# Performance work log

Measured on AMD Instinct MI355X. Metric: run time of the kernel, lower is better.

The kernel has to match this reference:

```python
import jax, jax.numpy as jnp
import numpy as np
from jax.scipy.special import logsumexp

# static problem sizes (all graphs identical size; pairs interleaved [q0,c0,q1,c1,...])
B = 64; NG = 2 * B; N = 48; E = 192; MAX_N = 64; MAX_E = 256
D_IN = 32; D = 128; EDGE_EMB = 128; M = 256; S = 64
T = 5; K = 3; TEMP = 0.1; SINK_ITERS = 10
VN = NG * N; VE = NG * E


def _mlp2(x, W1, b1, W2, b2):
    return jnp.maximum(x @ W1 + b1, 0.0) @ W2 + b2


def setup_inputs():
    keys = iter(jax.random.split(jax.random.key(0), 64))
    def w(fan_in, fan_out):
        return jax.random.normal(next(keys), (fan_in, fan_out), dtype=jnp.float32) * (1.0 / float(np.sqrt(fan_in)))
    z = lambda n: jnp.zeros((n,), jnp.float32)
    inp = {}
    inp['node_features'] = jax.random.normal(next(keys), (VN, D_IN), dtype=jnp.float32)
    inp['edge_features'] = jax.random.normal(next(keys), (VE, D_IN), dtype=jnp.float32)
    off = jnp.repeat(jnp.arange(NG, dtype=jnp.int32) * N, E)
    inp['from_idx'] = jax.random.randint(next(keys), (VE,), 0, N, dtype=jnp.int32) + off
    inp['to_idx'] = jax.random.randint(next(keys), (VE,), 0, N, dtype=jnp.int32) + off
    inp['enc_node_W'] = w(D_IN, D); inp['enc_node_b'] = z(D)
    inp['enc_edge_W'] = w(D_IN, EDGE_EMB); inp['enc_edge_b'] = z(EDGE_EMB)
    inp['ni_W1'] = w(2 * D, 2 * D); inp['ni_b1'] = z(2 * D)
    inp['ni_W2'] = w(2 * D, D); inp['ni_b2'] = z(D)
    ei_in = M + EDGE_EMB
    inp['ei_W1'] = w(ei_in, ei_in); inp['ei_b1'] = z(ei_in)
    inp['ei_W2'] = w(ei_in, EDGE_EMB); inp['ei_b2'] = z(EDGE_EMB)
    inp['msg_W'] = w(2 * D + EDGE_EMB, M); inp['msg_b'] = z(M)
    inp['nu_W1'] = w(D + M, 2 * D); inp['nu_b1'] = z(2 * D)
    inp['nu_W2'] = w(2 * D, D); inp['nu_b2'] = z(D)
    inp['ns_W1'] = w(D, S); inp['ns_b1'] = z(S)
    inp['ns_W2'] = w(S, S); inp['ns_b2'] = z(S)
    inp['es_W1'] = w(M, S); inp['es_b1'] = z(S)
    inp['es_W2'] = w(S, S); inp['es_b2'] = z(S)
    return inp


def _forward(node_features, edge_features, enc_node_W, enc_node_b, enc_edge_W, enc_edge_b,
             ni_W1, ni_b1, ni_W2, ni_b2, ei_W1, ei_b1, ei_W2, ei_b2, msg_W, msg_b,
             nu_W1, nu_b1, nu_W2, nu_b2, ns_W1, ns_b1, ns_W2, ns_b2,
             es_W1, es_b1, es_W2, es_b2, from_idx, to_idx):
    enc_n = node_features @ enc_node_W + enc_node_b            # [VN, D]
    enc_e = edge_features @ enc_edge_W + enc_edge_b            # [VE, EDGE_EMB]
    node_store = jnp.zeros((VN, D * (T + 1)), jnp.float32)
    edge_store = jnp.zeros((VE, M * (T + 1)), jnp.float32)
    # flat index of node/edge j of graph g inside interleaved padded store: g*max + j
    node_pad_idx = (jnp.arange(NG)[:, None] * MAX_N + jnp.arange(N)[None, :]).reshape(-1)
    edge_pad_idx = (jnp.arange(NG)[:, None] * MAX_E + jnp.arange(E)[None, :]).reshape(-1)
    node_mask = (jnp.arange(MAX_N) < N).astype(jnp.float32)[None, :, None]
    edge_mask = (jnp.arange(MAX_E) < E).astype(jnp.float32)[None, :, None]

    def transport(store, n_per, max_set, fdim, sW1, sb1, sW2, sb2, mask):
        x = store.reshape(NG, n_per, store.shape[-1])
        x = jnp.pad(x, ((0, 0), (0, max_set - n_per), (0, 0)))   # pad to max set size
        q, c = x[0::2], x[1::2]                                   # [B, max, dim_total]
        fq, fc = q[:, :, -fdim:], c[:, :, -fdim:]
        tq = _mlp2(fq, sW1, sb1, sW2, sb2) * mask
        tc = _mlp2(fc, sW1, sb1, sW2, sb2) * mask
        la = jnp.einsum('bqs,bcs->bqc', tq, tc) / TEMP
        for _ in range(SINK_ITERS):
            la = la - logsumexp(la, axis=2, keepdims=True)
            la = la - logsumexp(la, axis=1, keepdims=True)
        plan = jnp.exp(la)
        qi = jnp.einsum('bqc,bcd->bqd', plan, c)                  # query <- corpus
        ci = jnp.einsum('bqc,bqd->bcd', plan, q)                  # corpus <- query
        inter = jnp.stack([qi, ci], axis=1).reshape(NG * max_set, -1)
        return plan, inter, fq, fc

    for _ in range(K):  # time_update_steps
        h, e = enc_n, enc_e
        node_slots = [jnp.zeros((VN, D), jnp.float32)]
        edge_slots = [jnp.zeros((VE, M), jnp.float32)]
        for p in range(1, T + 1):  # propagation_steps
            h_comb = _mlp2(jnp.concatenate([h, node_store[:, (p - 1) * D:p * D]], -1), ni_W1, ni_b1, ni_W2, ni_b2)
            e_comb = _mlp2(jnp.concatenate([e, edge_store[:, (p - 1) * M:p * M]], -1), ei_W1, ei_b1, ei_W2, ei_b2)
            src, dst = h_comb[from_idx], h_comb[to_idx]
            fwd_msg = jnp.concatenate([src, dst, e_comb], -1) @ msg_W + msg_b
            bwd_msg = jnp.concatenate([dst, src, e_comb], -1) @ msg_W + msg_b
            agg = jax.ops.segment_sum(fwd_msg, to_idx, num_segments=VN) + jax.ops.segment_sum(bwd_msg, from_idx, num_segments=VN)
            h = _mlp2(jnp.concatenate([h_comb, agg], -1), nu_W1, nu_b1, nu_W2, nu_b2)
            src2, dst2 = h[from_idx], h[to_idx]
            msgs = (jnp.concatenate([src2, dst2, e_comb], -1) @ msg_W + msg_b) + \
                   (jnp.concatenate([dst2, src2, e_comb], -1) @ msg_W + msg_b)
            node_slots.append(h)
            edge_slots.append(msgs)
        upd_node = jnp.concatenate(node_slots, axis=1)
        upd_edge = jnp.concatenate(edge_slots, axis=1)
        n_plan, n_inter, ffq, ffc = transport(upd_node, N, MAX_N, D, ns_W1, ns_b1, ns_W2, ns_b2, node_mask)
        _, e_inter, _, _ = transport(upd_edge, E, MAX_E, M, es_W1, es_b1, es_W2, es_b2, edge_mask)
        node_store = jnp.concatenate([jnp.zeros((VN, D), jnp.float32), n_inter[node_pad_idx, D:]], axis=1)
        edge_store = jnp.concatenate([jnp.zeros((VE, M), jnp.float32), e_inter[edge_pad_idx, M:]], axis=1)

    # feature_alignment_score: -sum relu(q - P c)
    score = -jnp.sum(jnp.maximum(ffq - jnp.einsum('bqc,bcd->bqd', n_plan, ffc), 0.0), axis=(1, 2))
    return score


def reference(node_features, edge_features, from_idx, to_idx, enc_node_W, enc_node_b, enc_edge_W, enc_edge_b,
              ni_W1, ni_b1, ni_W2, ni_b2, ei_W1, ei_b1, ei_W2, ei_b2, msg_W, msg_b,
              nu_W1, nu_b1, nu_W2, nu_b2, ns_W1, ns_b1, ns_W2, ns_b2,
              es_W1, es_b1, es_W2, es_b2):
    return _forward(node_features, edge_features, enc_node_W, enc_node_b, enc_edge_W, enc_edge_b,
                    ni_W1, ni_b1, ni_W2, ni_b2, ei_W1, ei_b1, ei_W2, ei_b2, msg_W, msg_b,
                    nu_W1, nu_b1, nu_W2, nu_b2, ns_W1, ns_b1, ns_W2, ns_b2,
                    es_W1, es_b1, es_W2, es_b2, from_idx, to_idx)
```

## Files before the change

### kernel.cpp

```cpp
#include <hip/hip_runtime.h>
#include <cstdint>
#include <cstddef>

#define NGg   128
#define Bb    64
#define Nn    48
#define Ee    192
#define Sdim  64
#define VNn   6144
#define VEe   24576
#define INV_TEMP 10.0f
#define ADJ_STRIDE 96

typedef unsigned short u16;
typedef unsigned int   u32;
typedef __attribute__((ext_vector_type(8))) short short8;
typedef __attribute__((ext_vector_type(4))) float floatx4;

__device__ __forceinline__ u16 f2bf(float f)
{
    unsigned int u = __float_as_uint(f);
    u += 0x7FFFu + ((u >> 16) & 1u);
    return (u16)(u >> 16);
}
// ... 233 lines not shown
            for (int q = 0; q < 8; q++) {
                hi[q] = __builtin_amdgcn_perm(pk[2 * q + 1], pk[2 * q], 0x05040100u);
                lo[q] = __builtin_amdgcn_perm(pk[2 * q + 1], pk[2 * q], 0x07060302u);
            }
            *(uint4*)&Ah[srow * TW + skoff]     = ((uint4*)hi)[0];
            *(uint4*)&Ah[srow * TW + skoff + 8] = ((uint4*)hi)[1];
            *(uint4*)&Al[srow * TW + skoff]     = ((uint4*)lo)[0];
            *(uint4*)&Al[srow * TW + skoff + 8] = ((uint4*)lo)[1];
        }
        __syncthreads();
        short8 afh[4], afl[4], bfh[4], bfl[4];
        #pragma unroll
        for (int i = 0; i < 4; i++) {
            const int ro = (wm * 64 + i * 16 + l15) * TW + lq * 8;
            afh[i] = *(const short8*)&Ah[ro];
            afl[i] = *(const short8*)&Al[ro];
        }
        #pragma unroll
        for (int j = 0; j < 4; j++) {
            const int ro = (wn * 64 + j * 16 + l15) * TW + lq * 8;
            bfh[j] = *(const short8*)&Bh[ro];
            bfl[j] = *(const short8*)&Bl[ro];
        }
        #pragma unroll
        for (int i = 0; i < 4; i++)
            #pragma unroll
            for (int j = 0; j < 4; j++) {
                acc[i][j] = __builtin_amdgcn_mfma_f32_16x16x32_bf16(afh[i], bfl[j], acc[i][j], 0, 0, 0);
                acc[i][j] = __builtin_amdgcn_mfma_f32_16x16x32_bf16(afl[i], bfh[j], acc[i][j], 0, 0, 0);
                acc[i][j] = __builtin_amdgcn_mfma_f32_16x16x32_bf16(afh[i], bfh[j], acc[i][j], 0, 0, 0);
            }
        __syncthreads();
    }
    if (d.flags & FL_MSGS) {
        #pragma unroll
        for (int i = 0; i < 4; i++) {
            #pragma unroll
            for (int r = 0; r < 4; r++) {
                const int row = bm + wm * 64 + i * 16 + lq * 4 + r;
                const int fi = d.fidx[row], ti = d.tidx[row];
                #pragma unroll
                for (int j = 0; j < 4; j++) {
                    const int col = bn + wn * 64 + j * 16 + l15;
                    float v = 2.f * (acc[i][j][r] + d.bias[col])
                            + d.qs[(size_t)fi * 256 + col] + d.qs[(size_t)ti * 256 + col];
                    ((u32*)d.C)[(size_t)row * d.ldc + col] = packhl(v);
                }
            }
        }
        return;
    }
    const int relu = d.flags & FL_RELU;
    const int opk  = d.flags & FL_OUTPK;
    #pragma unroll
    for (int j = 0; j < 4; j++) {
        const int col = bn + wn * 64 + j * 16 + l15;
        const bool cok = (col < d.Ncap);
        const float bv = (d.bias && cok) ? d.bias[col] : 0.f;
        #pragma unroll
        for (int i = 0; i < 4; i++) {
            const int row0 = bm + wm * 64 + i * 16 + lq * 4;
            #pragma unroll
            for (int r = 0; r < 4; r++) {
                float v = acc[i][j][r] + bv;
                if (relu) v = fmaxf(v, 0.f);
                if (cok) {
                    if (opk)
                        ((u32*)d.C)[(size_t)(row0 + r) * d.ldc + col] = packhl(v);
                    else
                        ((float*)d.C)[(size_t)(row0 + r) * d.ldc + col] = v;
                }
            }
        }
    }
}

static inline void gemm2(hipStream_t s, const GemmDesc& d0, const GemmDesc& d1)
{
    gemm2_pk_kernel<<<d0.nblk + d1.nblk, 256, 0, s>>>(d0, d1, d0.nblk);
}
static inline void gemm1(hipStream_t s, const GemmDesc& d0)
{
    gemm2_pk_kernel<<<d0.nblk, 256, 0, s>>>(d0, d0, d0.nblk);
}

__global__ __launch_bounds__(256) void gemm_f32_kernel(
    const float* __restrict__ A, int lda, int K,
    const u16* __restrict__ Wh, const u16* __restrict__ Wl, int ldwt,
    const float* __restrict__ bias, u32* __restrict__ C, int ldc, int Ncap)
{
    __shared__ __align__(16) u16 Ah[128 * TW];
    __shared__ __align__(16) u16 Al[128 * TW];
    __shared__ __align__(16) u16 Bh[128 * TW];
    __shared__ __align__(16) u16 Bl[128 * TW];
    const int tid = threadIdx.x;
    const int lane = tid & 63, wave = tid >> 6;
    const int wm = wave >> 1, wn = wave & 1;
    const int bm = blockIdx.y * 128, bn = blockIdx.x * 128;
    const int srow = tid >> 1;
    const int skoff = (tid & 1) * 16;
    const int arow = bm + srow, brow = bn + srow;
    const int l15 = lane & 15, lq = lane >> 4;

    floatx4 acc[4][4];
    #pragma unroll
    for (int i = 0; i < 4; i++)
        #pragma unroll
        for (int j = 0; j < 4; j++) acc[i][j] = (floatx4){0.f, 0.f, 0.f, 0.f};

    for (int k0 = 0; k0 < K; k0 += 32) {
        const int kk = k0 + skoff;
        const float* asrc = A + (size_t)arow * lda + kk;
        float f[16];
        ((float4*)f)[0] = ((const float4*)asrc)[0];
        ((float4*)f)[1] = ((const float4*)asrc)[1];
        ((float4*)f)[2] = ((const float4*)asrc)[2];
        ((float4*)f)[3] = ((const float4*)asrc)[3];
        u16 ph[16], pl8[16];
        #pragma unroll
        for (int q = 0; q < 16; q++) {
            u16 h = f2bf(f[q]);
            ph[q] = h;
            pl8[q] = f2bf(f[q] - bf2f(h));
        }
        *(uint4*)&Ah[srow * TW + skoff]     = *(const uint4*)&ph[0];
        *(uint4*)&Ah[srow * TW + skoff + 8] = *(const uint4*)&ph[8];
        *(uint4*)&Al[srow * TW + skoff]     = *(const uint4*)&pl8[0];
        *(uint4*)&Al[srow * TW + skoff + 8] = *(const uint4*)&pl8[8];
        const u16* bh = Wh + (size_t)brow * ldwt + kk;
        const u16* bl = Wl + (size_t)brow * ldwt + kk;
        *(uint4*)&Bh[srow * TW + skoff]     = ((const uint4*)bh)[0];
        *(uint4*)&Bh[srow * TW + skoff + 8] = ((const uint4*)bh)[1];
        *(uint4*)&Bl[srow * TW + skoff]     = ((const uint4*)bl)[0];
        *(uint4*)&Bl[srow * TW + skoff + 8] = ((const uint4*)bl)[1];
        __syncthreads();
        short8 afh[4], afl[4], bfh[4], bfl[4];
        #pragma unroll
        for (int i = 0; i < 4; i++) {
            const int ro = (wm * 64 + i * 16 + l15) * TW + lq * 8;
            afh[i] = *(const short8*)&Ah[ro];
            afl[i] = *(const short8*)&Al[ro];
        }
        #pragma unroll
        for (int j = 0; j < 4; j++) {
            const int ro = (wn * 64 + j * 16 + l15) * TW + lq * 8;
            bfh[j] = *(const short8*)&Bh[ro];
            bfl[j] = *(const short8*)&Bl[ro];
        }
        #pragma unroll
        for (int i = 0; i < 4; i++)
            #pragma unroll
            for (int j = 0; j < 4; j++) {
                acc[i][j] = __builtin_amdgcn_mfma_f32_16x16x32_bf16(afh[i], bfl[j], acc[i][j], 0, 0, 0);
                acc[i][j] = __builtin_amdgcn_mfma_f32_16x16x32_bf16(afl[i], bfh[j], acc[i][j], 0, 0, 0);
                acc[i][j] = __builtin_amdgcn_mfma_f32_16x16x32_bf16(afh[i], bfh[j], acc[i][j], 0, 0, 0);
            }
        __syncthreads();
    }
    #pragma unroll
    for (int j = 0; j < 4; j++) {
        const int col = bn + wn * 64 + j * 16 + l15;
        const bool cok = (col < Ncap);
        const float bv = cok ? bias[col] : 0.f;
        #pragma unroll
        for (int i = 0; i < 4; i++) {
            const int row0 = bm + wm * 64 + i * 16 + lq * 4;
// ... 92 lines not shown
                } else {
                    #pragma unroll
                    for (int i = 0; i < 8; i++)
                        pk[i] = Pb[(size_t)(k0 + sak + i) * ms + m];
                }
                #pragma unroll
                for (int i = 0; i < 8; i++)
                    if (k0 + sak + i >= n_per) pk[i] = 0;
            } else {
                #pragma unroll
                for (int i = 0; i < 8; i++) pk[i] = 0;
            }
            u32 hi[4], lo[4];
            #pragma unroll
            for (int q = 0; q < 4; q++) {
                hi[q] = __builtin_amdgcn_perm(pk[2 * q + 1], pk[2 * q], 0x05040100u);
                lo[q] = __builtin_amdgcn_perm(pk[2 * q + 1], pk[2 * q], 0x07060302u);
            }
            *(uint4*)&Ah[sar * TW + sak] = *(uint4*)hi;
            *(uint4*)&Al[sar * TW + sak] = *(uint4*)lo;
        }
        {
            u16 qh[16], ql[16];
            #pragma unroll
            for (int i = 0; i < 16; i++) {
                int kk = k0 + sbk + i;
                u32 w = 0;
                if (kk < n_per) w = U[(size_t)(ibase + kk) * ldu + bn + sbn];
                qh[i] = (u16)w; ql[i] = (u16)(w >> 16);
            }
            *(uint4*)&Bh[sbn * TW + sbk]     = *(const uint4*)&qh[0];
            *(uint4*)&Bh[sbn * TW + sbk + 8] = *(const uint4*)&qh[8];
            *(uint4*)&Bl[sbn * TW + sbk]     = *(const uint4*)&ql[0];
            *(uint4*)&Bl[sbn * TW + sbk + 8] = *(const uint4*)&ql[8];
        }
        __syncthreads();
        short8 afh[2], afl[2], bfh[4], bfl[4];
        #pragma unroll
        for (int i = 0; i < 2; i++) {
            const int ro = (wm * 32 + i * 16 + l15) * TW + lq * 8;
            afh[i] = *(const short8*)&Ah[ro];
            afl[i] = *(const short8*)&Al[ro];
        }
        #pragma unroll
        for (int j = 0; j < 4; j++) {
            const int ro = (wn * 64 + j * 16 + l15) * TW + lq * 8;
            bfh[j] = *(const short8*)&Bh[ro];
            bfl[j] = *(const short8*)&Bl[ro];
        }
        #pragma unroll
        for (int i = 0; i < 2; i++)
            #pragma unroll
            for (int j = 0; j < 4; j++) {
                acc[i][j] = __builtin_amdgcn_mfma_f32_16x16x32_bf16(afh[i], bfl[j], acc[i][j], 0, 0, 0);
                acc[i][j] = __builtin_amdgcn_mfma_f32_16x16x32_bf16(afl[i], bfh[j], acc[i][j], 0, 0, 0);
                acc[i][j] = __builtin_amdgcn_mfma_f32_16x16x32_bf16(afh[i], bfh[j], acc[i][j], 0, 0, 0);
            }
        __syncthreads();
    }
    #pragma unroll
    for (int j = 0; j < 4; j++) {
        const int col = bn + wn * 64 + j * 16 + l15;
        #pragma unroll
        for (int i = 0; i < 2; i++) {
            const int row0 = bm + wm * 32 + i * 16 + lq * 4;
            #pragma unroll
            for (int r = 0; r < 4; r++) {
                const int m = row0 + r;
                if (m < n_per)
                    C[(size_t)(obase + m) * ldc + col] = packhl(acc[i][j][r]);
            }
        }
    }
}

static inline void bgemmDual(hipStream_t s, const u32* P, int ms, int n_per,
                             const u32* U, int ldu, u32* C, int ldc, int N)
{
    int nxh = N / 128;
    dim3 grid(nxh * 2, (n_per + 63) / 64, Bb);
    bgemm_dual_kernel<<<grid, 256, 0, s>>>(P, ms, n_per, U, ldu, C, ldc, nxh);
}

__global__ __launch_bounds__(256) void la_sinkhorn64_kernel(
    const float* __restrict__ tt, u32* __restrict__ n_la)
{
    const int b = blockIdx.x;
    __shared__ float Aq[64][65];
    __shared__ float Ac[64][65];
    __shared__ float m[64][65];
    __shared__ float v_s[64];
    __shared__ float part[4][64];
    const int tid = threadIdx.x;
    const int lane = tid & 63, w = tid >> 6;
    for (int idx = tid; idx < 4096; idx += 256) {
        int r = idx >> 6, s = idx & 63;
        float vq = 0.f, vc = 0.f;
        if (r < Nn) {
            vq = tt[((size_t)(2 * b) * Nn + r) * Sdim + s];
            vc = tt[((size_t)(2 * b + 1) * Nn + r) * Sdim + s];
        }
        Aq[r][s] = vq;
        Ac[r][s] = vc;
    }
    __syncthreads();
    {
        const int tx = tid & 15, ty = tid >> 4;
        float acc[4][4] = {};
        for (int s = 0; s < 64; s++) {
            float a[4], c[4];
            #pragma unroll
            for (int i = 0; i < 4; i++) a[i] = Aq[ty * 4 + i][s];
            #pragma unroll
            for (int j = 0; j < 4; j++) c[j] = Ac[tx * 4 + j][s];
            #pragma unroll
            for (int i = 0; i < 4; i++)
                #pragma unroll
                for (int j = 0; j < 4; j++)
                    acc[i][j] = fmaf(a[i], c[j], acc[i][j]);
        }
        #pragma unroll
        for (int i = 0; i < 4; i++)
            #pragma unroll
            for (int j = 0; j < 4; j++)
                m[ty * 4 + i][tx * 4 + j] = acc[i][j] * INV_TEMP;
    }
    if (tid < 64) v_s[tid] = 0.f;
    __syncthreads();
    float x[16], u[16];
    #pragma unroll
    for (int j = 0; j < 16; j++) x[j] = m[w * 16 + j][lane];
    #pragma unroll
    for (int j = 0; j < 16; j++) {
        float mx = x[j];
        #pragma unroll
        for (int d = 1; d < 64; d <<= 1) mx = fmaxf(mx, __shfl_xor(mx, d));
        u[j] = mx;
    }
    for (int it = 0; it < 10; it++) {
        float vr = v_s[lane];
        #pragma unroll
        for (int j = 0; j < 16; j++) {
            float s = __expf(x[j] - vr - u[j]);
            #pragma unroll
            for (int d = 1; d < 64; d <<= 1) s += __shfl_xor(s, d);
            u[j] += __logf(s);
        }
        float s = 0.f;
        #pragma unroll
        for (int j = 0; j < 16; j++) s += __expf(x[j] - u[j] - vr);
        part[w][lane] = s;
        __syncthreads();
        if (tid < 64) {
            float ss = part[0][tid] + part[1][tid] + part[2][tid] + part[3][tid];
            v_s[tid] += __logf(ss);
        }
        __syncthreads();
    }
    float vr = v_s[lane];
    u32* g = n_la + (size_t)b * 4096;
    #pragma unroll
    for (int j = 0; j < 16; j++)
        g[(size_t)(w * 16 + j) * 64 + lane] = packhl(__expf(x[j] - u[j] - vr));
}

__global__ __launch_bounds__(256) void la_gemm256_kernel(
    const float* __restrict__ tt, float* __restrict__ la)
{
    const int b = blockIdx.z;
    const int bm = blockIdx.y * 64, bn = blockIdx.x * 64;
    __shared__ float Aq[64][65];
    __shared__ float Ac[64][65];
    const int tid = threadIdx.x;
    for (int idx = tid; idx < 4096; idx += 256) {
        int r = idx >> 6, s = idx & 63;
        float vq = 0.f, vc = 0.f;
        int qr = bm + r, cr = bn + r;
        if (qr < Ee) vq = tt[((size_t)(2 * b) * Ee + qr) * Sdim + s];
        if (cr < Ee) vc = tt[((size_t)(2 * b + 1) * Ee + cr) * Sdim + s];
        Aq[r][s] = vq;
        Ac[r][s] = vc;
    }
    __syncthreads();
    const int tx = tid & 15, ty = tid >> 4;
    float acc[4][4] = {};
    for (int s = 0; s < 64; s++) {
        float a[4], c[4];
        #pragma unroll
        for (int i = 0; i < 4; i++) a[i] = Aq[ty * 4 + i][s];
        #pragma unroll
        for (int j = 0; j < 4; j++) c[j] = Ac[tx * 4 + j][s];
        #pragma unroll
        for (int i = 0; i < 4; i++)
            #pragma unroll
            for (int j = 0; j < 4; j++)
                acc[i][j] = fmaf(a[i], c[j], acc[i][j]);
    }
    #pragma unroll
    for (int i = 0; i < 4; i++)
        #pragma unroll
        for (int j = 0; j < 4; j++)
            la[((size_t)b * 256 + bm + ty * 4 + i) * 256 + bn + tx * 4 + j] = acc[i][j] * INV_TEMP;
}

__global__ __launch_bounds__(1024, 4) void sinkhorn256_kernel(float* __restrict__ la)
{
    const int b = blockIdx.x;
    float* g = la + (size_t)b * 65536;
    const int tid = threadIdx.x;
    const int lane = tid & 63, w = tid >> 6;
    __shared__ float v_s[256];
    __shared__ float part[16][64][5];

    float4 x[16];
    float u[16];
    #pragma unroll
    for (int j = 0; j < 16; j++) {
        x[j] = ((const float4*)(g + (size_t)(w * 16 + j) * 256))[lane];
        float mx = fmaxf(fmaxf(x[j].x, x[j].y), fmaxf(x[j].z, x[j].w));
        #pragma unroll
        for (int d = 1; d < 64; d <<= 1) mx = fmaxf(mx, __shfl_xor(mx, d));
        u[j] = mx;
    }
    if (tid < 256) v_s[tid] = 0.f;
    __syncthreads();

    for (int it = 0; it < 10; it++) {
        const float4 vr = *(const float4*)&v_s[4 * lane];
        float cp0 = 0.f, cp1 = 0.f, cp2 = 0.f, cp3 = 0.f;
        #pragma unroll
        for (int j = 0; j < 16; j++) {
            float e0 = __expf(x[j].x - vr.x - u[j]);
            float e1 = __expf(x[j].y - vr.y - u[j]);
            float e2 = __expf(x[j].z - vr.z - u[j]);
            float e3 = __expf(x[j].w - vr.w - u[j]);
            float s = e0 + e1 + e2 + e3;
            #pragma unroll
            for (int d = 1; d < 64; d <<= 1) s += __shfl_xor(s, d);
            u[j] += __logf(s);
            const float inv = 1.f / s;
            cp0 = fmaf(e0, inv, cp0);
            cp1 = fmaf(e1, inv, cp1);
            cp2 = fmaf(e2, inv, cp2);
            cp3 = fmaf(e3, inv, cp3);
        }
        *(float4*)&part[w][lane][0] = (float4){cp0, cp1, cp2, cp3};
        __syncthreads();
        if (tid < 256) {
            const int cl = tid >> 2, cq = tid & 3;
            float ss = 0.f;
            #pragma unroll
            for (int w2 = 0; w2 < 16; w2++) ss += part[w2][cl][cq];
            v_s[tid] += __logf(ss);
        }
        __syncthreads();
    }
    const float4 vr = *(const float4*)&v_s[4 * lane];
    #pragma unroll
    for (int j = 0; j < 16; j++) {
        u32 o[4];
        o[0] = packhl(__expf(x[j].x - u[j] - vr.x));
        o[1] = packhl(__expf(x[j].y - u[j] - vr.y));
        o[2] = packhl(__expf(x[j].z - u[j] - vr.z));
        o[3] = packhl(__expf(x[j].w - u[j] - vr.w));
        ((uint4*)(g + (size_t)(w * 16 + j) * 256))[lane] = *(uint4*)o;
    }
}

__global__ __launch_bounds__(256) void zero_deg_kernel(int* __restrict__ deg)
{
    deg[blockIdx.x * 256 + threadIdx.x] = 0;
}

__global__ __launch_bounds__(256) void csr_build_kernel(
    const int* __restrict__ from_idx, const int* __restrict__ to_idx,
    int* __restrict__ deg, u32* __restrict__ adj)
{
    int e = blockIdx.x * 256 + threadIdx.x;
    if (e >= VEe) return;
    int f = from_idx[e], t = to_idx[e];
    int p1 = atomicAdd(&deg[t], 1);
    if (p1 < ADJ_STRIDE) adj[(size_t)t * ADJ_STRIDE + p1] = ((u32)e << 13) | (u32)f;
    int p2 = atomicAdd(&deg[f], 1);
    if (p2 < ADJ_STRIDE) adj[(size_t)f * ADJ_STRIDE + p2] = ((u32)e << 13) | (u32)t;
}

__global__ __launch_bounds__(256) void agg_csr_kernel(
    const u32* __restrict__ P01,
    const u32* __restrict__ ec2,
    const int* __restrict__ deg, const u32* __restrict__ adj,
    u32* __restrict__ agg)
{
    const int n = blockIdx.x;
    const int d = threadIdx.x;
    __shared__ u32 sadj[ADJ_STRIDE];
    __shared__ int sdeg;
    if (d == 0) sdeg = min(deg[n], ADJ_STRIDE);
    if (d < ADJ_STRIDE) sadj[d] = adj[(size_t)n * ADJ_STRIDE + d];
    __syncthreads();
    const int dn = sdeg;
    float a = (float)dn * unpackhl(P01[(size_t)n * 512 + 256 + d]);
    for (int i = 0; i < dn; i++) {
        const u32 en = sadj[i];
        const int e = (int)(en >> 13), pr = (int)(en & 8191u);
        a += unpackhl(ec2[(size_t)e * 256 + d]) + unpackhl(P01[(size_t)pr * 512 + d]);
    }
    agg[(size_t)n * 256 + d] = packhl(a);
}

__global__ __launch_bounds__(256) void msgs_inplace_kernel(
    u32* __restrict__ m, const float* __restrict__ Qs,
    const int* __restrict__ from_idx, const int* __restrict__ to_idx)
{
    const int e = blockIdx.x;
    const int d = threadIdx.x;
    const int f = from_idx[e], t = to_idx[e];
    size_t o = (size_t)e * 256 + d;
    float v = Qs[(size_t)f * 256 + d] + Qs[(size_t)t * 256 + d] + 2.f * unpackhl(m[o]);
    m[o] = packhl(v);
}

__global__ void diag_kernel(float* __restrict__ out, float v)
{
    out[threadIdx.x] = v;
}

__global__ __launch_bounds__(128) void score_kernel(
    const u32* __restrict__ upd_node, const u32* __restrict__ plan,
    float* __restrict__ out)
{
    const int b = blockIdx.x;
    const int tid = threadIdx.x;
    __shared__ float ffc[48][128];
    __shared__ float pl[64][48];
    __shared__ float red[128];
    for (int c = 0; c < 48; c++)
        ffc[c][tid] = unpackhl(upd_node[(size_t)((2 * b + 1) * 48 + c) * 640 + 512 + tid]);
    for (int idx = tid; idx < 64 * 48; idx += 128) {
        int q = idx / 48, c = idx % 48;
        pl[q][c] = unpackhl(plan[(size_t)b * 4096 + q * 64 + c]);
    }
    __syncthreads();
    float accv = 0.f;
    for (int q = 0; q < 64; q++) {
        float rsum = 0.f;
        #pragma unroll 8
        for (int c = 0; c < 48; c++) rsum = fmaf(pl[q][c], ffc[c][tid], rsum);
        float fq = 0.f;
        if (q < 48) fq = unpackhl(upd_node[(size_t)((2 * b) * 48 + q) * 640 + 512 + tid]);
        accv += fmaxf(fq - rsum, 0.f);
    }
    red[tid] = accv;
    __syncthreads();
    for (int sft = 64; sft > 0; sft >>= 1) {
        if (tid < sft) red[tid] += red[tid + sft];
        __syncthreads();
    }
    if (tid == 0) out[b] = -red[0];
}

#define OFF_UPD_NODE   0ULL
#define OFF_NODE_STORE 3932160ULL
#define OFF_EDGE_STORE 7077888ULL
#define OFF_ECOMB      32243712ULL
#define OFF_ENC_N      47972352ULL
#define OFF_ENC_E      48758784ULL
#define OFF_N_LA       51904512ULL
#define OFF_WT         52199424ULL
#define OFF_WTL        52547584ULL
#define OFF_ARENA      52895744ULL
#define OFF_DEG        66265088ULL
#define OFF_ADJ        66271232ULL
#define TOTAL_FLOATS   66861056ULL

#define WT_NIW1   0
#define WT_NIW2   65536
#define WT_EIW1   98304
#define WT_EIW2   245760
#define WT_MSG    294912
#define WT_P01    393216
#define WT_NUW1   458752
#define WT_NUW2   557056
#define WT_WSUM   589824
#define WT_ENCN   622592
#define WT_ENCE   626688
#define WT_NS1    630784
#define WT_NS2    647168
#define WT_ES1    655360
#define WT_ES2    688128

#define PK(p) ((u32*)(p))

extern "C" void kernel_launch(void* const* d_in, const int* in_sizes, int n_in,
                              void* d_out, int out_size, void* d_ws, size_t ws_size,
                              hipStream_t stream)
{
    (void)in_sizes; (void)n_in; (void)out_size;
    if (ws_size < TOTAL_FLOATS * sizeof(float)) {
        diag_kernel<<<1, 64, 0, stream>>>((float*)d_out, (float)ws_size);
        return;
    }

// ... 34 lines not shown
    float* edge_store = ws + OFF_EDGE_STORE;
    float* ecomb      = ws + OFF_ECOMB;
    float* enc_n      = ws + OFF_ENC_N;
    float* enc_e      = ws + OFF_ENC_E;
    float* n_la       = ws + OFF_N_LA;
    u16* WT  = (u16*)(ws + OFF_WT);
    u16* WTL = (u16*)(ws + OFF_WTL);
    float* arena      = ws + OFF_ARENA;
    int* deg = (int*)(ws + OFF_DEG);
    u32* adj = (u32*)(ws + OFF_ADJ);

    float* A_hidden = arena;
    float* A_hcomb  = arena + 1572864;
    float* A_ehid   = arena + 2359296;
    float* A_ec2    = arena + 2359296;
    float* A_P01    = arena + 8650752;
    float* A_aggb   = arena + 11796480;
    float* B_Qs       = arena;
    float* B_Qs2      = ecomb + (size_t)4 * VEe * 128;
    float* B_thid_e   = arena + 8650752;
    float* B_ttreal_e = arena + 10223616;
    float* B_ela      = arena + 2359296;
    float* B_msgs     = arena + 6553600;
    float* B_thid_n   = arena + 12058624;
    float* B_ttreal_n = arena + 12451840;

    prep_kernel<<<(696320 + 255) / 256, 256, 0, stream>>>(
        ni_W1, ni_W2, ei_W1, ei_W2, msg_W, nu_W1, nu_W2,
        enc_node_W, enc_edge_W, ns_W1, ns_W2, es_W1, es_W2, WT, WTL);
    zero_deg_kernel<<<VNn / 256, 256, 0, stream>>>(deg);
    csr_build_kernel<<<VEe / 256, 256, 0, stream>>>(from_idx, to_idx, deg, adj);

    gemm_f32_kernel<<<dim3(1, VNn / 128), 256, 0, stream>>>(
        node_features, 32, 32, WT + WT_ENCN, WTL + WT_ENCN, 32, enc_node_b, PK(enc_n), 128, 128);
    gemm_f32_kernel<<<dim3(1, VEe / 128), 256, 0, stream>>>(
        edge_features, 32, 32, WT + WT_ENCE, WTL + WT_ENCE, 32, enc_edge_b, PK(enc_e), 128, 128);

    for (int k = 0; k < 3; k++) {
        for (int p = 1; p <= 5; p++) {
            const bool hs = (k > 0) && (p > 1);
            const u32* hA1 = (p == 1) ? PK(enc_n) : PK(upd_node + (size_t)(p - 2) * 128);
            const int  hlda1 = (p == 1) ? 128 : 640;
            const u32* hA2 = hs ? PK(node_store + (size_t)(p - 2) * 128) : nullptr;
            const int  hK2 = hs ? 128 : 0;
            GemmDesc hcomb1_d = mkDesc(hA1, hlda1, 128, hA2, 512, hK2,
                                       WT + WT_NIW1, WTL + WT_NIW1, 256, ni_b1,
                                       A_hidden, 256, VNn, 256, 256, FL_RELU | FL_OUTPK);
            GemmDesc hcomb2_d = mkDesc(PK(A_hidden), 256, 256, nullptr, 0, 0,
                                       WT + WT_NIW2, WTL + WT_NIW2, 256, ni_b2,
                                       A_hcomb, 128, VNn, 128, 128, FL_OUTPK);
            GemmDesc p01_d = mkDesc(PK(A_hcomb), 128, 128, nullptr, 0, 0,
                                    WT + WT_P01, WTL + WT_P01, 128, nullptr,
                                    A_P01, 512, VNn, 512, 512, FL_OUTPK);

            const bool edge_full = ((k == 0 && p == 1) || (k > 0 && p > 1));
            if (edge_full) {
                const u32* esrc = (k == 0) ? nullptr : PK(edge_store + (size_t)(p - 2) * 256);
                const int  eK2  = (k == 0) ? 0 : 256;
                float* ec_slot = (k == 0) ? ecomb : ecomb + (size_t)(p - 1) * VEe * 128;
                GemmDesc eiW1_d = mkDesc(PK(enc_e), 128, 128, esrc, 1024, eK2,
                                         WT + WT_EIW1, WTL + WT_EIW1, 384, ei_b1,
                                         A_ehid, 384, VEe, 384, 384, FL_RELU | FL_OUTPK);
                GemmDesc eiW2_d = mkDesc(PK(A_ehid), 384, 384, nullptr, 0, 0,
                                         WT + WT_EIW2, WTL + WT_EIW2, 384, ei_b2,
                                         ec_slot, 128, VEe, 128, 128, FL_OUTPK);
                GemmDesc ec2_d = mkDesc(PK(ec_slot), 128, 128, nullptr, 0, 0,
                                        WT + WT_MSG + 256, WTL + WT_MSG + 256, 384, msg_b,
                                        A_ec2, 256, VEe, 256, 256, FL_OUTPK);
                gemm2(stream, eiW1_d, hcomb1_d);
                gemm2(stream, eiW2_d, hcomb2_d);
                gemm2(stream, ec2_d, p01_d);
            } else if (k > 0 && p == 1) {
                GemmDesc ec2_d = mkDesc(PK(ecomb), 128, 128, nullptr, 0, 0,
                                        WT + WT_MSG + 256, WTL + WT_MSG + 256, 384, msg_b,
                                        A_ec2, 256, VEe, 256, 256, FL_OUTPK);
                gemm2(stream, ec2_d, hcomb1_d);
                gemmPK(stream, 64, 64, PK(A_hidden), 256, 256, nullptr, 0, 0,
                       WT + WT_NIW2, WTL + WT_NIW2, 256,
                       ni_b2, A_hcomb, 128, VNn, 128, 128, FL_OUTPK);
                gemmPK(stream, 64, 128, PK(A_hcomb), 128, 128, nullptr, 0, 0,
                       WT + WT_P01, WTL + WT_P01, 128,
                       nullptr, A_P01, 512, VNn, 512, 512, FL_OUTPK);
            } else {
                gemmPK(stream, 64, 128, hA1, hlda1, 128, hA2, 512, hK2,
                       WT + WT_NIW1, WTL + WT_NIW1, 256, ni_b1,
                       A_hidden, 256, VNn, 256, 256, FL_RELU | FL_OUTPK);
                gemmPK(stream, 64, 64, PK(A_hidden), 256, 256, nullptr, 0, 0,
                       WT + WT_NIW2, WTL + WT_NIW2, 256,
                       ni_b2, A_hcomb, 128, VNn, 128, 128, FL_OUTPK);
                gemmPK(stream, 64, 128, PK(A_hcomb), 128, 128, nullptr, 0, 0,
                       WT + WT_P01, WTL + WT_P01, 128,
                       nullptr, A_P01, 512, VNn, 512, 512, FL_OUTPK);
            }
            agg_csr_kernel<<<VNn, 256, 0, stream>>>(PK(A_P01), PK(A_ec2), deg, adj, PK(A_aggb));
            gemmPK(stream, 64, 128, PK(A_hcomb), 128, 128, PK(A_aggb), 256, 256,
                   WT + WT_NUW1, WTL + WT_NUW1, 384,
                   nu_b1, A_hidden, 256, VNn, 256, 256, FL_RELU | FL_OUTPK);
            gemmPK(stream, 64, 64, PK(A_hidden), 256, 256, nullptr, 0, 0,
                   WT + WT_NUW2, WTL + WT_NUW2, 256,
                   nu_b2, upd_node + (size_t)(p - 1) * 128, 640, VNn, 128, 128, FL_OUTPK);
        }
        if (k < 2) {
            gemmPK(stream, 64, 128, PK(upd_node + 512), 640, 128, nullptr, 0, 0,
                   WT + WT_WSUM, WTL + WT_WSUM, 128,
                   nullptr, B_Qs, 256, VNn, 256, 256, 0);
            msgs_inplace_kernel<<<VEe, 256, 0, stream>>>(PK(A_ec2), B_Qs, from_idx, to_idx);
            GemmDesc es1_d = mkDesc(PK(A_ec2), 256, 256, nullptr, 0, 0,
                                    WT + WT_ES1, WTL + WT_ES1, 256, es_b1,
                                    B_thid_e, 64, VEe, 128, 64, FL_RELU | FL_OUTPK);
            GemmDesc ns1_d = mkDesc(PK(upd_node + 512), 640, 128, nullptr, 0, 0,
                                    WT + WT_NS1, WTL + WT_NS1, 128, ns_b1,
                                    B_thid_n, 64, VNn, 128, 64, FL_RELU | FL_OUTPK);
            gemm2(stream, es1_d, ns1_d);
            GemmDesc es2_d = mkDesc(PK(B_thid_e), 64, 64, nullptr, 0, 0,
                                    WT + WT_ES2, WTL + WT_ES2, 64, es_b2,
                                    B_ttreal_e, 64, VEe, 128, 64, 0);
            GemmDesc ns2_d = mkDesc(PK(B_thid_n), 64, 64, nullptr, 0, 0,
                                    WT + WT_NS2, WTL + WT_NS2, 64, ns_b2,
                                    B_ttreal_n, 64, VNn, 128, 64, 0);
            gemm2(stream, es2_d, ns2_d);
            la_sinkhorn64_kernel<<<Bb, 256, 0, stream>>>(B_ttreal_n, PK(n_la));
            la_gemm256_kernel<<<dim3(4, 4, Bb), 256, 0, stream>>>(B_ttreal_e, B_ela);
            sinkhorn256_kernel<<<Bb, 1024, 0, stream>>>(B_ela);
            bgemmDual(stream, PK(n_la), 64, 48, PK(upd_node), 640, PK(node_store), 512, 512);
            float* qsbuf[2] = { B_Qs2, B_Qs };
            GemmDesc qs1_d = mkDesc(PK(upd_node), 640, 128, nullptr, 0, 0,
                                    WT + WT_WSUM, WTL + WT_WSUM, 128, nullptr,
                                    qsbuf[0], 256, VNn, 256, 256, 0);
            gemm1(stream, qs1_d);
            for (int sl = 1; sl <= 4; sl++) {
                const size_t ss = (k == 0) ? 0 : (size_t)(sl - 1);
                GemmDesc em_d = mkDesc(PK(ecomb + ss * VEe * 128), 128, 128, nullptr, 0, 0,
                                       WT + WT_MSG + 256, WTL + WT_MSG + 256, 384, msg_b,
                                       B_msgs, 256, VEe, 256, 256, FL_MSGS);
                em_d.qs = qsbuf[(sl - 1) & 1];
                em_d.fidx = from_idx; em_d.tidx = to_idx;
                if (sl < 4) {
                    GemmDesc qsn_d = mkDesc(PK(upd_node + (size_t)sl * 128), 640, 128,
                                            nullptr, 0, 0,
                                            WT + WT_WSUM, WTL + WT_WSUM, 128, nullptr,
                                            qsbuf[sl & 1], 256, VNn, 256, 256, 0);
                    gemm2(stream, em_d, qsn_d);
                } else {
                    gemm1(stream, em_d);
                }
                bgemmDual(stream, PK(B_ela), 256, 192, PK(B_msgs), 256,
                          PK(edge_store + (size_t)(sl - 1) * 256), 1024, 256);
            }
        } else {
            gemmPK(stream, 64, 64, PK(upd_node + 512), 640, 128, nullptr, 0, 0,
                   WT + WT_NS1, WTL + WT_NS1, 128,
                   ns_b1, B_thid_n, 64, VNn, 64, 64, FL_RELU | FL_OUTPK);
            gemmPK(stream, 64, 64, PK(B_thid_n), 64, 64, nullptr, 0, 0,
                   WT + WT_NS2, WTL + WT_NS2, 64,
                   ns_b2, B_ttreal_n, 64, VNn, 64, 64, 0);
            la_sinkhorn64_kernel<<<Bb, 256, 0, stream>>>(B_ttreal_n, PK(n_la));
        }
    }
    score_kernel<<<Bb, 128, 0, stream>>>(PK(upd_node), PK(n_la), (float*)d_out);
}
```

Measured before the change: 2.916 ms.

## Fuse message construction into ES1 GEMM, merge LA kernels, retune tiles

Adds a dedicated GEMM kernel that builds the edge message (Qs[from]+Qs[to]+2*ec2) on the fly while loading A tiles, which removes the separate in-place message kernel and its full read/write pass over the edge buffer. The Qs GEMM is now batched with the NS1 GEMM in one launch. The node Sinkhorn and edge logit GEMM kernels are merged into one launch distinguished by block index. The 256 Sinkhorn kernel now re-reads rows from global memory each iteration instead of holding them in registers, and drops its occupancy hint, trading memory traffic for register pressure. Some node GEMM tile widths change from 128 to 64.

```diff
diff --git a/kernel.cpp b/kernel.cpp
--- a/kernel.cpp
+++ b/kernel.cpp
@@ -339,6 +339,111 @@
 static inline void gemm1(hipStream_t s, const GemmDesc& d0)
 {
     gemm2_pk_kernel<<<d0.nblk, 256, 0, s>>>(d0, d0, d0.nblk);
+}
+
+__global__ __launch_bounds__(256) void gemm_es1msgs_kernel(
+    const u32* __restrict__ A,
+    const float* __restrict__ qs,
+    const int* __restrict__ fidx, const int* __restrict__ tidx,
+    const u16* __restrict__ Wh, const u16* __restrict__ Wl,
+    const float* __restrict__ bias,
+    u32* __restrict__ C)
+{
+    __shared__ __align__(16) u16 Ah[128 * TW];
+    __shared__ __align__(16) u16 Al[128 * TW];
+    __shared__ __align__(16) u16 Bh[64 * TW];
+    __shared__ __align__(16) u16 Bl[64 * TW];
+    const int tid = threadIdx.x;
+    const int lane = tid & 63, wave = tid >> 6;
+    const int wm = wave >> 1, wn = wave & 1;
+    const int bm = blockIdx.y * 128;
+    const int AR = tid >> 1, AKo = (tid & 1) * 16;
+    const int BR = tid >> 2, BKo = (tid & 3) * 8;
+    const int arow = bm + AR;
+    const int l15 = lane & 15, lq = lane >> 4;
+    const int fi = fidx[arow], ti = tidx[arow];
+
+    floatx4 acc[4][2];
+    #pragma unroll
+    for (int i = 0; i < 4; i++)
+        #pragma unroll
+        for (int j = 0; j < 2; j++) acc[i][j] = (floatx4){0.f, 0.f, 0.f, 0.f};
+
+    for (int k0 = 0; k0 < 256; k0 += 32) {
+        {
+            const int kk = k0 + BKo;
+            const u16* bh = Wh + (size_t)BR * 256 + kk;
+            const u16* bl = Wl + (size_t)BR * 256 + kk;
+            *(uint4*)&Bh[BR * TW + BKo] = ((const uint4*)bh)[0];
+            *(uint4*)&Bl[BR * TW + BKo] = ((const uint4*)bl)[0];
+        }
+        {
+            const int kk = k0 + AKo;
+            const u32* asrc = A + (size_t)arow * 256 + kk;
+            u32 pk[16];
+            ((uint4*)pk)[0] = ((const uint4*)asrc)[0];
+            ((uint4*)pk)[1] = ((const uint4*)asrc)[1];
+            ((uint4*)pk)[2] = ((const uint4*)asrc)[2];
+            ((uint4*)pk)[3] = ((const uint4*)asrc)[3];
+            float qf[16], qt[16];
+            const float* qfp = qs + (size_t)fi * 256 + kk;
+            const float* qtp = qs + (size_t)ti * 256 + kk;
+            #pragma unroll
+            for (int q = 0; q < 4; q++) {
+                ((float4*)qf)[q] = ((const float4*)qfp)[q];
+                ((float4*)qt)[q] = ((const float4*)qtp)[q];
+            }
+            u16 ph[16], pl8[16];
+            #pragma unroll
+            for (int q = 0; q < 16; q++) {
+                float v = qf[q] + qt[q] + 2.f * unpackhl(pk[q]);
+                u16 h = f2bf(v);
+                ph[q] = h;
+                pl8[q] = f2bf(v - bf2f(h));
+            }
+            *(uint4*)&Ah[AR * TW + AKo]     = *(const uint4*)&ph[0];
+            *(uint4*)&Ah[AR * TW + AKo + 8] = *(const uint4*)&ph[8];
+            *(uint4*)&Al[AR * TW + AKo]     = *(const uint4*)&pl8[0];
+            *(uint4*)&Al[AR * TW + AKo + 8] = *(const uint4*)&pl8[8];
+        }
+        __syncthreads();
+        short8 afh[4], afl[4], bfh[2], bfl[2];
+        #pragma unroll
+        for (int i = 0; i < 4; i++) {
+            const int ro = (wm * 64 + i * 16 + l15) * TW + lq * 8;
+            afh[i] = *(const short8*)&Ah[ro];
+            afl[i] = *(const short8*)&Al[ro];
+        }
+        #pragma unroll
+        for (int j = 0; j < 2; j++) {
+            const int ro = (wn * 32 + j * 16 + l15) * TW + lq * 8;
+            bfh[j] = *(const short8*)&Bh[ro];
+            bfl[j] = *(const short8*)&Bl[ro];
+        }
+        #pragma unroll
+        for (int i = 0; i < 4; i++)
+            #pragma unroll
+            for (int j = 0; j < 2; j++) {
+                acc[i][j] = __builtin_amdgcn_mfma_f32_16x16x32_bf16(afh[i], bfl[j], acc[i][j], 0, 0, 0);
+                acc[i][j] = __builtin_amdgcn_mfma_f32_16x16x32_bf16(afl[i], bfh[j], acc[i][j], 0, 0, 0);
+                acc[i][j] = __builtin_amdgcn_mfma_f32_16x16x32_bf16(afh[i], bfh[j], acc[i][j], 0, 0, 0);
+            }
+        __syncthreads();
+    }
+    #pragma unroll
+    for (int j = 0; j < 2; j++) {
+        const int col = wn * 32 + j * 16 + l15;
+        const float bv = bias[col];
+        #pragma unroll
+        for (int i = 0; i < 4; i++) {
+            const int row0 = bm + wm * 64 + i * 16 + lq * 4;
+            #pragma unroll
+            for (int r = 0; r < 4; r++) {
+                float v = fmaxf(acc[i][j][r] + bv, 0.f);
+                C[(size_t)(row0 + r) * 64 + col] = packhl(v);
+            }
+        }
+    }
 }
 
 __global__ __launch_bounds__(256) void gemm_f32_kernel(
@@ -597,23 +702,59 @@
     bgemm_dual_kernel<<<grid, 256, 0, s>>>(P, ms, n_per, U, ldu, C, ldc, nxh);
 }
 
-__global__ __launch_bounds__(256) void la_sinkhorn64_kernel(
-    const float* __restrict__ tt, u32* __restrict__ n_la)
-{
-    const int b = blockIdx.x;
+__global__ __launch_bounds__(256) void la_fused_kernel(
+    const float* __restrict__ ttn, u32* __restrict__ n_la,
+    const float* __restrict__ tte, float* __restrict__ ela)
+{
     __shared__ float Aq[64][65];
     __shared__ float Ac[64][65];
     __shared__ float m[64][65];
     __shared__ float v_s[64];
     __shared__ float part[4][64];
     const int tid = threadIdx.x;
+    if ((int)blockIdx.x >= 64) {
+        const int id = blockIdx.x - 64;
+        const int b = id >> 4;
+        const int bm = ((id >> 2) & 3) * 64, bn = (id & 3) * 64;
+        for (int idx = tid; idx < 4096; idx += 256) {
+            int r = idx >> 6, s = idx & 63;
+            float vq = 0.f, vc = 0.f;
+            int qr = bm + r, cr = bn + r;
+            if (qr < Ee) vq = tte[((size_t)(2 * b) * Ee + qr) * Sdim + s];
+            if (cr < Ee) vc = tte[((size_t)(2 * b + 1) * Ee + cr) * Sdim + s];
+            Aq[r][s] = vq;
+            Ac[r][s] = vc;
+        }
+        __syncthreads();
+        const int tx = tid & 15, ty = tid >> 4;
+        float acc[4][4] = {};
+        for (int s = 0; s < 64; s++) {
+            float a[4], c[4];
+            #pragma unroll
+            for (int i = 0; i < 4; i++) a[i] = Aq[ty * 4 + i][s];
+            #pragma unroll
+            for (int j = 0; j < 4; j++) c[j] = Ac[tx * 4 + j][s];
+            #pragma unroll
+            for (int i = 0; i < 4; i++)
+                #pragma unroll
+                for (int j = 0; j < 4; j++)
+                    acc[i][j] = fmaf(a[i], c[j], acc[i][j]);
+        }
+        #pragma unroll
+        for (int i = 0; i < 4; i++)
+            #pragma unroll
+            for (int j = 0; j < 4; j++)
+                ela[((size_t)b * 256 + bm + ty * 4 + i) * 256 + bn + tx * 4 + j] = acc[i][j] * INV_TEMP;
+        return;
+    }
+    const int b = blockIdx.x;
     const int lane = tid & 63, w = tid >> 6;
     for (int idx = tid; idx < 4096; idx += 256) {
         int r = idx >> 6, s = idx & 63;
         float vq = 0.f, vc = 0.f;
         if (r < Nn) {
-            vq = tt[((size_t)(2 * b) * Nn + r) * Sdim + s];
-            vc = tt[((size_t)(2 * b + 1) * Nn + r) * Sdim + s];
+            vq = ttn[((size_t)(2 * b) * Nn + r) * Sdim + s];
+            vc = ttn[((size_t)(2 * b + 1) * Nn + r) * Sdim + s];
         }
         Aq[r][s] = vq;
         Ac[r][s] = vc;
@@ -679,46 +820,7 @@
         g[(size_t)(w * 16 + j) * 64 + lane] = packhl(__expf(x[j] - u[j] - vr));
 }
 
-__global__ __launch_bounds__(256) void la_gemm256_kernel(
-    const float* __restrict__ tt, float* __restrict__ la)
-{
-    const int b = blockIdx.z;
-    const int bm = blockIdx.y * 64, bn = blockIdx.x * 64;
-    __shared__ float Aq[64][65];
-    __shared__ float Ac[64][65];
-    const int tid = threadIdx.x;
-    for (int idx = tid; idx < 4096; idx += 256) {
-        int r = idx >> 6, s = idx & 63;
-        float vq = 0.f, vc = 0.f;
-        int qr = bm + r, cr = bn + r;
-        if (qr < Ee) vq = tt[((size_t)(2 * b) * Ee + qr) * Sdim + s];
-        if (cr < Ee) vc = tt[((size_t)(2 * b + 1) * Ee + cr) * Sdim + s];
-        Aq[r][s] = vq;
-        Ac[r][s] = vc;
-    }
-    __syncthreads();
-    const int tx = tid & 15, ty = tid >> 4;
-    float acc[4][4] = {};
-    for (int s = 0; s < 64; s++) {
-        float a[4], c[4];
-        #pragma unroll
-        for (int i = 0; i < 4; i++) a[i] = Aq[ty * 4 + i][s];
-        #pragma unroll
-        for (int j = 0; j < 4; j++) c[j] = Ac[tx * 4 + j][s];
-        #pragma unroll
-        for (int i = 0; i < 4; i++)
-            #pragma unroll
-            for (int j = 0; j < 4; j++)
-                acc[i][j] = fmaf(a[i], c[j], acc[i][j]);
-    }
-    #pragma unroll
-    for (int i = 0; i < 4; i++)
-        #pragma unroll
-        for (int j = 0; j < 4; j++)
-            la[((size_t)b * 256 + bm + ty * 4 + i) * 256 + bn + tx * 4 + j] = acc[i][j] * INV_TEMP;
-}
-
-__global__ __launch_bounds__(1024, 4) void sinkhorn256_kernel(float* __restrict__ la)
+__global__ __launch_bounds__(1024) void sinkhorn256_kernel(float* __restrict__ la)
 {
     const int b = blockIdx.x;
     float* g = la + (size_t)b * 65536;
@@ -727,12 +829,11 @@
     __shared__ float v_s[256];
     __shared__ float part[16][64][5];
 
-    float4 x[16];
     float u[16];
     #pragma unroll
     for (int j = 0; j < 16; j++) {
-        x[j] = ((const float4*)(g + (size_t)(w * 16 + j) * 256))[lane];
-        float mx = fmaxf(fmaxf(x[j].x, x[j].y), fmaxf(x[j].z, x[j].w));
+        float4 xv = ((const float4*)(g + (size_t)(w * 16 + j) * 256))[lane];
+        float mx = fmaxf(fmaxf(xv.x, xv.y), fmaxf(xv.z, xv.w));
         #pragma unroll
         for (int d = 1; d < 64; d <<= 1) mx = fmaxf(mx, __shfl_xor(mx, d));
         u[j] = mx;
@@ -745,10 +846,11 @@
         float cp0 = 0.f, cp1 = 0.f, cp2 = 0.f, cp3 = 0.f;
         #pragma unroll
         for (int j = 0; j < 16; j++) {
-            float e0 = __expf(x[j].x - vr.x - u[j]);
-            float e1 = __expf(x[j].y - vr.y - u[j]);
-            float e2 = __expf(x[j].z - vr.z - u[j]);
-            float e3 = __expf(x[j].w - vr.w - u[j]);
+            float4 xv = ((const float4*)(g + (size_t)(w * 16 + j) * 256))[lane];
+            float e0 = __expf(xv.x - vr.x - u[j]);
+            float e1 = __expf(xv.y - vr.y - u[j]);
+            float e2 = __expf(xv.z - vr.z - u[j]);
+            float e3 = __expf(xv.w - vr.w - u[j]);
             float s = e0 + e1 + e2 + e3;
             #pragma unroll
             for (int d = 1; d < 64; d <<= 1) s += __shfl_xor(s, d);
@@ -773,12 +875,14 @@
     const float4 vr = *(const float4*)&v_s[4 * lane];
     #pragma unroll
     for (int j = 0; j < 16; j++) {
+        float4* rp = (float4*)(g + (size_t)(w * 16 + j) * 256) + lane;
+        float4 xv = *rp;
         u32 o[4];
-        o[0] = packhl(__expf(x[j].x - u[j] - vr.x));
-        o[1] = packhl(__expf(x[j].y - u[j] - vr.y));
-        o[2] = packhl(__expf(x[j].z - u[j] - vr.z));
-        o[3] = packhl(__expf(x[j].w - u[j] - vr.w));
-        ((uint4*)(g + (size_t)(w * 16 + j) * 256))[lane] = *(uint4*)o;
+        o[0] = packhl(__expf(xv.x - u[j] - vr.x));
+        o[1] = packhl(__expf(xv.y - u[j] - vr.y));
+        o[2] = packhl(__expf(xv.z - u[j] - vr.z));
+        o[3] = packhl(__expf(xv.w - u[j] - vr.w));
+        *(uint4*)rp = *(uint4*)o;
     }
 }
 
@@ -821,18 +925,6 @@
         a += unpackhl(ec2[(size_t)e * 256 + d]) + unpackhl(P01[(size_t)pr * 512 + d]);
     }
     agg[(size_t)n * 256 + d] = packhl(a);
-}
-
-__global__ __launch_bounds__(256) void msgs_inplace_kernel(
-    u32* __restrict__ m, const float* __restrict__ Qs,
-    const int* __restrict__ from_idx, const int* __restrict__ to_idx)
-{
-    const int e = blockIdx.x;
-    const int d = threadIdx.x;
-    const int f = from_idx[e], t = to_idx[e];
-    size_t o = (size_t)e * 256 + d;
-    float v = Qs[(size_t)f * 256 + d] + Qs[(size_t)t * 256 + d] + 2.f * unpackhl(m[o]);
-    m[o] = packhl(v);
 }
 
 __global__ void diag_kernel(float* __restrict__ out, float v)
@@ -1033,7 +1125,7 @@
                        WT + WT_P01, WTL + WT_P01, 128,
                        nullptr, A_P01, 512, VNn, 512, 512, FL_OUTPK);
             } else {
-                gemmPK(stream, 64, 128, hA1, hlda1, 128, hA2, 512, hK2,
+                gemmPK(stream, 64, 64, hA1, hlda1, 128, hA2, 512, hK2,
                        WT + WT_NIW1, WTL + WT_NIW1, 256, ni_b1,
                        A_hidden, 256, VNn, 256, 256, FL_RELU | FL_OUTPK);
                 gemmPK(stream, 64, 64, PK(A_hidden), 256, 256, nullptr, 0, 0,
@@ -1044,7 +1136,7 @@
                        nullptr, A_P01, 512, VNn, 512, 512, FL_OUTPK);
             }
             agg_csr_kernel<<<VNn, 256, 0, stream>>>(PK(A_P01), PK(A_ec2), deg, adj, PK(A_aggb));
-            gemmPK(stream, 64, 128, PK(A_hcomb), 128, 128, PK(A_aggb), 256, 256,
+            gemmPK(stream, 64, 64, PK(A_hcomb), 128, 128, PK(A_aggb), 256, 256,
                    WT + WT_NUW1, WTL + WT_NUW1, 384,
                    nu_b1, A_hidden, 256, VNn, 256, 256, FL_RELU | FL_OUTPK);
             gemmPK(stream, 64, 64, PK(A_hidden), 256, 256, nullptr, 0, 0,
@@ -1052,17 +1144,16 @@
                    nu_b2, upd_node + (size_t)(p - 1) * 128, 640, VNn, 128, 128, FL_OUTPK);
         }
         if (k < 2) {
-            gemmPK(stream, 64, 128, PK(upd_node + 512), 640, 128, nullptr, 0, 0,
-                   WT + WT_WSUM, WTL + WT_WSUM, 128,
-                   nullptr, B_Qs, 256, VNn, 256, 256, 0);
-            msgs_inplace_kernel<<<VEe, 256, 0, stream>>>(PK(A_ec2), B_Qs, from_idx, to_idx);
-            GemmDesc es1_d = mkDesc(PK(A_ec2), 256, 256, nullptr, 0, 0,
-                                    WT + WT_ES1, WTL + WT_ES1, 256, es_b1,
-                                    B_thid_e, 64, VEe, 128, 64, FL_RELU | FL_OUTPK);
+            GemmDesc qs_d = mkDesc(PK(upd_node + 512), 640, 128, nullptr, 0, 0,
+                                   WT + WT_WSUM, WTL + WT_WSUM, 128, nullptr,
+                                   B_Qs, 256, VNn, 256, 256, 0);
             GemmDesc ns1_d = mkDesc(PK(upd_node + 512), 640, 128, nullptr, 0, 0,
                                     WT + WT_NS1, WTL + WT_NS1, 128, ns_b1,
                                     B_thid_n, 64, VNn, 128, 64, FL_RELU | FL_OUTPK);
-            gemm2(stream, es1_d, ns1_d);
+            gemm2(stream, qs_d, ns1_d);
+            gemm_es1msgs_kernel<<<dim3(1, VEe / 128), 256, 0, stream>>>(
+                PK(A_ec2), B_Qs, from_idx, to_idx,
+                WT + WT_ES1, WTL + WT_ES1, es_b1, PK(B_thid_e));
             GemmDesc es2_d = mkDesc(PK(B_thid_e), 64, 64, nullptr, 0, 0,
                                     WT + WT_ES2, WTL + WT_ES2, 64, es_b2,
                                     B_ttreal_e, 64, VEe, 128, 64, 0);
@@ -1070,8 +1161,7 @@
                                     WT + WT_NS2, WTL + WT_NS2, 64, ns_b2,
                                     B_ttreal_n, 64, VNn, 128, 64, 0);
             gemm2(stream, es2_d, ns2_d);
-            la_sinkhorn64_kernel<<<Bb, 256, 0, stream>>>(B_ttreal_n, PK(n_la));
-            la_gemm256_kernel<<<dim3(4, 4, Bb), 256, 0, stream>>>(B_ttreal_e, B_ela);
+            la_fused_kernel<<<64 + 1024, 256, 0, stream>>>(B_ttreal_n, PK(n_la), B_ttreal_e, B_ela);
             sinkhorn256_kernel<<<Bb, 1024, 0, stream>>>(B_ela);
             bgemmDual(stream, PK(n_la), 64, 48, PK(upd_node), 640, PK(node_store), 512, 512);
             float* qsbuf[2] = { B_Qs2, B_Qs };
@@ -1105,7 +1195,7 @@
             gemmPK(stream, 64, 64, PK(B_thid_n), 64, 64, nullptr, 0, 0,
                    WT + WT_NS2, WTL + WT_NS2, 64,
                    ns_b2, B_ttreal_n, 64, VNn, 64, 64, 0);
-            la_sinkhorn64_kernel<<<Bb, 256, 0, stream>>>(B_ttreal_n, PK(n_la));
+            la_fused_kernel<<<64, 256, 0, stream>>>(B_ttreal_n, PK(n_la), B_ttreal_e, B_ela);
         }
     }
     score_kernel<<<Bb, 128, 0, stream>>>(PK(upd_node), PK(n_la), (float*)d_out);
```

Measured after the change: 2.943 ms. Within noise of the previous version (+0.9%).
